# Performance work log

Hardware: AMD Instinct MI355X
Metric: run time of the kernel (lower is better)

The kernel has to match this reference:

```python
import jax, jax.numpy as jnp
import numpy as np

B, F, H, S, K, L, C = 128, 8192, 8192, 4, 32, 3, 100  # batch, encoded feats, hidden, segments, synapses/seg, hidden layers, classes


def setup_inputs() -> dict:
    key = jax.random.key(0)
    k1, k2, k3, k4, k5, k6 = jax.random.split(key, 6)
    # binary encoded input activations (thermometer-coded tabular features)
    x = jax.random.randint(k1, (B, F), 0, 2).astype(jnp.float32)
    # sign weights in {-1,+1} for each synapse of each segment of each neuron
    signs0 = jnp.where(jax.random.bernoulli(k2, 0.5, (S, H, K)), 1.0, -1.0).astype(jnp.float32)
    signsH = jnp.where(jax.random.bernoulli(k3, 0.5, (L - 1, S, H, K)), 1.0, -1.0).astype(jnp.float32)
    # synapse source indices (irregular connectivity)
    idx0 = jax.random.randint(k4, (S, H, K), 0, F, dtype=jnp.int32)
    idxH = jax.random.randint(k5, (L - 1, S, H, K), 0, H, dtype=jnp.int32)
    # per-layer output connection matrices [L, H, C]
    wout = jax.random.normal(k6, (L, H, C), dtype=jnp.float32) * 0.02
    return {"x": x, "signs0": signs0, "signsH": signsH, "wout": wout,
            "idx0": idx0, "idxH": idxH, "threshold": 8}


def _segment_layer(a, idx, signs, threshold):
    # a: [B, P] prev activations; idx/signs: [S, H, K]
    g = a[:, idx]                                  # [B, S, H, K] irregular gather
    z = jnp.einsum('bshk,shk->bsh', g, signs)      # per-segment summed input
    fired = jnp.any(z >= threshold, axis=1)        # OR over segments -> [B, H]
    return fired.astype(a.dtype)


def reference(x, signs0, signsH, wout, idx0, idxH, threshold):
    thr = jnp.float32(threshold)
    a = _segment_layer(x, idx0, signs0, thr)       # hidden layer 0
    acts = [a]
    for l in range(idxH.shape[0]):                 # remaining hidden layers (fixed small L)
        a = _segment_layer(a, idxH[l], signsH[l], thr)
        acts.append(a)
    # sum class votes from every hidden layer's output connection matrix
    out = jnp.einsum('lbh,lhc->bc', jnp.stack(acts, 0), wout)  # [B, C]
    return out
```

## Files before the change

kernel.cpp:

```cpp
#include <hip/hip_runtime.h>
#include <stdint.h>

#define B 128
#define F 8192
#define H 8192
#define S 4
#define K 32
#define L 3
#define C 100

__global__ void pack_x_kernel(const float* __restrict__ x, uint64_t* __restrict__ xP,
                              float* __restrict__ out) {
    const int zi = blockIdx.x * 128 + threadIdx.x;
    if (zi < B * C) out[zi] = 0.0f;

    const int b = threadIdx.x;
    const int w = threadIdx.x >> 6;
    const int f0 = blockIdx.x * 32;
    const float4* xr = (const float4*)(x + (size_t)b * F + f0);
    for (int j = 0; j < 8; ++j) {
        const float4 v = xr[j];
        const uint64_t m0 = __ballot(v.x > 0.5f);
        const uint64_t m1 = __ballot(v.y > 0.5f);
        const uint64_t m2 = __ballot(v.z > 0.5f);
        const uint64_t m3 = __ballot(v.w > 0.5f);
        if ((threadIdx.x & 63) == 0) {
            const int f = f0 + 4 * j;
            xP[(size_t)w * F + f + 0] = m0;
            xP[(size_t)w * F + f + 1] = m1;
            xP[(size_t)w * F + f + 2] = m2;
            xP[(size_t)w * F + f + 3] = m3;
        }
    }
}

__device__ __forceinline__ int load_threshold(const int* p) {
    int v = *p;
    if (v >= (1 << 23)) v = (int)__int_as_float(v);
    return v;
}

__global__ void layer_kernel(const uint64_t* __restrict__ prevP,
                             const int* __restrict__ idx,
                             const float* __restrict__ signs,
                             uint64_t* __restrict__ outP,
                             const int* __restrict__ thrp) {
    __shared__ uint64_t tab[H];
    const int tid  = threadIdx.x;
    const int lane = tid & 63;
    const int s    = tid >> 6;
    const int w    = blockIdx.x & 1;
    const int hg   = blockIdx.x >> 1;
    const int h    = hg * 64 + lane;
    const int thr  = load_threshold(thrp);

    {
        const ulonglong2* src = (const ulonglong2*)(prevP + (size_t)w * H);
        ulonglong2* dst = (ulonglong2*)tab;
#pragma unroll
        for (int i = 0; i < 16; ++i)
            dst[i * 256 + tid] = src[i * 256 + tid];
    }
    __syncthreads();

    uint64_t A[6] = {0, 0, 0, 0, 0, 0};
    uint64_t P[6] = {0, 0, 0, 0, 0, 0};
    const int4*   irow = (const int4*)(idx   + ((size_t)s * H + h) * K);
    const float4* srow = (const float4*)(signs + ((size_t)s * H + h) * K);
#pragma unroll
    for (int kk = 0; kk < 8; ++kk) {
        const int4   i4 = irow[kk];
        const float4 s4 = srow[kk];
        const int   iv[4] = {i4.x, i4.y, i4.z, i4.w};
        const float sv[4] = {s4.x, s4.y, s4.z, s4.w};
#pragma unroll
        for (int j = 0; j < 4; ++j) {
            const uint64_t a  = tab[iv[j]];
            const uint64_t pm = (uint64_t)(int64_t)(~(__float_as_int(sv[j]) >> 31));
            uint64_t c = a;
#pragma unroll
            for (int i = 0; i < 6; ++i) { const uint64_t t = A[i]; A[i] = t ^ c; c = t & c; }
            c = a & pm;
#pragma unroll
            for (int i = 0; i < 6; ++i) { const uint64_t t = P[i]; P[i] = t ^ c; c = t & c; }
        }
    }

    uint64_t Y[7];
    {
        uint64_t c = 0;
#pragma unroll
        for (int i = 0; i < 7; ++i) {
            const uint64_t ai = (i < 6) ? A[i] : 0ull;
            const uint64_t bm = ((thr >> i) & 1) ? ~0ull : 0ull;
            const uint64_t t  = ai ^ bm;
            Y[i] = t ^ c;
            c = (ai & bm) | (t & c);
        }
    }
    uint64_t bw = 0;
#pragma unroll
    for (int i = 0; i < 7; ++i) {
        const uint64_t x = (i >= 1) ? P[i - 1] : 0ull;
        const uint64_t d = x ^ Y[i];
        bw = ((~x) & Y[i]) | ((~d) & bw);
    }
    const uint64_t fired = ~bw;

    __syncthreads();
    uint64_t* fsbuf = tab;
    fsbuf[s * 64 + lane] = fired;
    __syncthreads();
    if (s == 0) {
        const uint64_t f = fsbuf[lane] | fsbuf[64 + lane] |
                           fsbuf[128 + lane] | fsbuf[192 + lane];
        outP[(size_t)w * H + h] = f;
    }
}

#define NHC 16
#define HCH (H / NHC)

__global__ void final_kernel(const uint64_t* __restrict__ actP,
                             const float* __restrict__ wout,
                             float* __restrict__ out) {
    const int lane = threadIdx.x & 63;
    const int wid  = threadIdx.x >> 6;
    const int hc   = blockIdx.x & (NHC - 1);
    const int bg   = blockIdx.x / NHC;
    const int b    = bg * 4 + wid;
    const int word = b >> 6;
    const int bit  = b & 63;

    float acc0 = 0.0f, acc1 = 0.0f;
    const int c1 = 64 + lane;
    const bool c1v = (c1 < C);

    for (int l = 0; l < L; ++l) {
        const uint64_t* aT = actP + ((size_t)l * 2 + word) * H;
        const float* wl = wout + (size_t)l * H * C;
        for (int r = 0; r < HCH / 64; ++r) {
            const int hbase = hc * HCH + r * 64;
            const uint64_t m = aT[hbase + lane];
            uint64_t hm = __ballot((m >> bit) & 1ull);
            while (hm) {
                const int slot = __ffsll((unsigned long long)hm) - 1;
                hm &= hm - 1;
                const float* wr = wl + (size_t)(hbase + slot) * C;
                acc0 += wr[lane];
                if (c1v) acc1 += wr[c1];
            }
        }
    }
    atomicAdd(&out[b * C + lane], acc0);
    if (c1v) atomicAdd(&out[b * C + c1], acc1);
}

extern "C" void kernel_launch(void* const* d_in, const int* in_sizes, int n_in,
                              void* d_out, int out_size, void* d_ws, size_t ws_size,
                              hipStream_t stream) {
    const float* x      = (const float*)d_in[0];
    const float* signs0 = (const float*)d_in[1];
    const float* signsH = (const float*)d_in[2];
    const float* wout   = (const float*)d_in[3];
    const int*   idx0   = (const int*)d_in[4];
    const int*   idxH   = (const int*)d_in[5];
    const int*   thr    = (const int*)d_in[6];
    float* out = (float*)d_out;

    uint64_t* xP   = (uint64_t*)d_ws;
    uint64_t* actP = xP + (size_t)2 * F;

    pack_x_kernel<<<F / 32, 128, 0, stream>>>(x, xP, out);

    layer_kernel<<<256, 256, 0, stream>>>(xP, idx0, signs0, actP, thr);
    layer_kernel<<<256, 256, 0, stream>>>(actP, idxH, signsH,
                                          actP + (size_t)2 * H, thr);
    layer_kernel<<<256, 256, 0, stream>>>(actP + (size_t)2 * H,
                                          idxH + (size_t)S * H * K,
                                          signsH + (size_t)S * H * K,
                                          actP + (size_t)4 * H, thr);

    final_kernel<<<32 * NHC, 256, 0, stream>>>(actP, wout, out);
}
```

Measured before the change: 129.1 us.

## Repack activations as 32-bit words and stage packed idx/sign rows in LDS

Bit-packed activations switch from two 64-bit batch words to four 32-bit words, which halves the per-block LDS table and doubles the layer grid from 256 to 512 blocks. Each block now loads its idx and sign rows cooperatively and coalesced, packs each sign bit into bit 31 of the index, and stores them in a padded LDS array. Threads then read from LDS instead of doing strided per-thread global loads, and they issue 8 gathers ahead of the popcount adders. The cost is that idx/sign global traffic is now repeated across the 4 batch-word blocks, and the bit-serial counter work is spread over twice as many blocks.

```diff
diff --git a/kernel.cpp b/kernel.cpp
--- a/kernel.cpp
+++ b/kernel.cpp
@@ -9,13 +9,13 @@
 #define L 3
 #define C 100
 
-__global__ void pack_x_kernel(const float* __restrict__ x, uint64_t* __restrict__ xP,
+__global__ void pack_x_kernel(const float* __restrict__ x, uint32_t* __restrict__ xP,
                               float* __restrict__ out) {
     const int zi = blockIdx.x * 128 + threadIdx.x;
     if (zi < B * C) out[zi] = 0.0f;
 
     const int b = threadIdx.x;
-    const int w = threadIdx.x >> 6;
+    const int wv = threadIdx.x >> 6;
     const int f0 = blockIdx.x * 32;
     const float4* xr = (const float4*)(x + (size_t)b * F + f0);
     for (int j = 0; j < 8; ++j) {
@@ -26,10 +26,12 @@
         const uint64_t m3 = __ballot(v.w > 0.5f);
         if ((threadIdx.x & 63) == 0) {
             const int f = f0 + 4 * j;
-            xP[(size_t)w * F + f + 0] = m0;
-            xP[(size_t)w * F + f + 1] = m1;
-            xP[(size_t)w * F + f + 2] = m2;
-            xP[(size_t)w * F + f + 3] = m3;
+            uint32_t* lo = xP + (size_t)(2 * wv) * F;
+            uint32_t* hi = xP + (size_t)(2 * wv + 1) * F;
+            lo[f + 0] = (uint32_t)m0;  hi[f + 0] = (uint32_t)(m0 >> 32);
+            lo[f + 1] = (uint32_t)m1;  hi[f + 1] = (uint32_t)(m1 >> 32);
+            lo[f + 2] = (uint32_t)m2;  hi[f + 2] = (uint32_t)(m2 >> 32);
+            lo[f + 3] = (uint32_t)m3;  hi[f + 3] = (uint32_t)(m3 >> 32);
         }
     }
 }
@@ -40,80 +42,100 @@
     return v;
 }
 
-__global__ void layer_kernel(const uint64_t* __restrict__ prevP,
+__global__ void layer_kernel(const uint32_t* __restrict__ prevP,
                              const int* __restrict__ idx,
                              const float* __restrict__ signs,
-                             uint64_t* __restrict__ outP,
+                             uint32_t* __restrict__ outP,
                              const int* __restrict__ thrp) {
-    __shared__ uint64_t tab[H];
+    __shared__ uint32_t tab[H];
+    __shared__ uint32_t isg[S][64 * 33];
+    __shared__ uint32_t fbuf[256];
     const int tid  = threadIdx.x;
     const int lane = tid & 63;
-    const int s    = tid >> 6;
-    const int w    = blockIdx.x & 1;
-    const int hg   = blockIdx.x >> 1;
+    const int sw   = tid >> 6;
+    const int w    = blockIdx.x & 3;
+    const int hg   = blockIdx.x >> 2;
     const int h    = hg * 64 + lane;
     const int thr  = load_threshold(thrp);
 
     {
-        const ulonglong2* src = (const ulonglong2*)(prevP + (size_t)w * H);
-        ulonglong2* dst = (ulonglong2*)tab;
-#pragma unroll
-        for (int i = 0; i < 16; ++i)
+        const int4* src = (const int4*)(prevP + (size_t)w * H);
+        int4* dst = (int4*)tab;
+#pragma unroll
+        for (int i = 0; i < 8; ++i)
             dst[i * 256 + tid] = src[i * 256 + tid];
     }
+    {
+        const int hrow = tid >> 2;
+        const int k0   = (tid & 3) * 8;
+#pragma unroll
+        for (int s = 0; s < S; ++s) {
+            const int4*   ib = (const int4*)(idx   + ((size_t)s * H + hg * 64) * K);
+            const float4* sb = (const float4*)(signs + ((size_t)s * H + hg * 64) * K);
+            const int4   ia = ib[2 * tid],     ic = ib[2 * tid + 1];
+            const float4 sa = sb[2 * tid],     sc = sb[2 * tid + 1];
+            uint32_t* dst = &isg[s][hrow * 33 + k0];
+            dst[0] = (uint32_t)ia.x | ((uint32_t)__float_as_int(sa.x) & 0x80000000u);
+            dst[1] = (uint32_t)ia.y | ((uint32_t)__float_as_int(sa.y) & 0x80000000u);
+            dst[2] = (uint32_t)ia.z | ((uint32_t)__float_as_int(sa.z) & 0x80000000u);
+            dst[3] = (uint32_t)ia.w | ((uint32_t)__float_as_int(sa.w) & 0x80000000u);
+            dst[4] = (uint32_t)ic.x | ((uint32_t)__float_as_int(sc.x) & 0x80000000u);
+            dst[5] = (uint32_t)ic.y | ((uint32_t)__float_as_int(sc.y) & 0x80000000u);
+            dst[6] = (uint32_t)ic.z | ((uint32_t)__float_as_int(sc.z) & 0x80000000u);
+            dst[7] = (uint32_t)ic.w | ((uint32_t)__float_as_int(sc.w) & 0x80000000u);
+        }
+    }
     __syncthreads();
 
-    uint64_t A[6] = {0, 0, 0, 0, 0, 0};
-    uint64_t P[6] = {0, 0, 0, 0, 0, 0};
-    const int4*   irow = (const int4*)(idx   + ((size_t)s * H + h) * K);
-    const float4* srow = (const float4*)(signs + ((size_t)s * H + h) * K);
-#pragma unroll
-    for (int kk = 0; kk < 8; ++kk) {
-        const int4   i4 = irow[kk];
-        const float4 s4 = srow[kk];
-        const int   iv[4] = {i4.x, i4.y, i4.z, i4.w};
-        const float sv[4] = {s4.x, s4.y, s4.z, s4.w};
-#pragma unroll
-        for (int j = 0; j < 4; ++j) {
-            const uint64_t a  = tab[iv[j]];
-            const uint64_t pm = (uint64_t)(int64_t)(~(__float_as_int(sv[j]) >> 31));
-            uint64_t c = a;
-#pragma unroll
-            for (int i = 0; i < 6; ++i) { const uint64_t t = A[i]; A[i] = t ^ c; c = t & c; }
-            c = a & pm;
-#pragma unroll
-            for (int i = 0; i < 6; ++i) { const uint64_t t = P[i]; P[i] = t ^ c; c = t & c; }
-        }
-    }
-
-    uint64_t Y[7];
+    uint32_t A[6] = {0, 0, 0, 0, 0, 0};
+    uint32_t P[6] = {0, 0, 0, 0, 0, 0};
+    const uint32_t* row = &isg[sw][lane * 33];
+#pragma unroll
+    for (int jc = 0; jc < K; jc += 8) {
+        uint32_t iv[8];
+#pragma unroll
+        for (int j = 0; j < 8; ++j) iv[j] = row[jc + j];
+        uint32_t a[8];
+#pragma unroll
+        for (int j = 0; j < 8; ++j) a[j] = tab[iv[j] & 0xFFFF];
+#pragma unroll
+        for (int j = 0; j < 8; ++j) {
+            const uint32_t pm = ~(uint32_t)((int32_t)iv[j] >> 31);
+            uint32_t c = a[j];
+#pragma unroll
+            for (int i = 0; i < 6; ++i) { const uint32_t t = A[i]; A[i] = t ^ c; c = t & c; }
+            c = a[j] & pm;
+#pragma unroll
+            for (int i = 0; i < 6; ++i) { const uint32_t t = P[i]; P[i] = t ^ c; c = t & c; }
+        }
+    }
+
+    uint32_t Y[7];
     {
-        uint64_t c = 0;
+        uint32_t c = 0;
 #pragma unroll
         for (int i = 0; i < 7; ++i) {
-            const uint64_t ai = (i < 6) ? A[i] : 0ull;
-            const uint64_t bm = ((thr >> i) & 1) ? ~0ull : 0ull;
-            const uint64_t t  = ai ^ bm;
+            const uint32_t ai = (i < 6) ? A[i] : 0u;
+            const uint32_t bm = ((thr >> i) & 1) ? 0xFFFFFFFFu : 0u;
+            const uint32_t t  = ai ^ bm;
             Y[i] = t ^ c;
             c = (ai & bm) | (t & c);
         }
     }
-    uint64_t bw = 0;
+    uint32_t bw = 0;
 #pragma unroll
     for (int i = 0; i < 7; ++i) {
-        const uint64_t x = (i >= 1) ? P[i - 1] : 0ull;
-        const uint64_t d = x ^ Y[i];
-        bw = ((~x) & Y[i]) | ((~d) & bw);
-    }
-    const uint64_t fired = ~bw;
-
+        const uint32_t xx = (i >= 1) ? P[i - 1] : 0u;
+        const uint32_t d  = xx ^ Y[i];
+        bw = ((~xx) & Y[i]) | ((~d) & bw);
+    }
+    const uint32_t fired = ~bw;
+
+    fbuf[sw * 64 + lane] = fired;
     __syncthreads();
-    uint64_t* fsbuf = tab;
-    fsbuf[s * 64 + lane] = fired;
-    __syncthreads();
-    if (s == 0) {
-        const uint64_t f = fsbuf[lane] | fsbuf[64 + lane] |
-                           fsbuf[128 + lane] | fsbuf[192 + lane];
+    if (sw == 0) {
+        const uint32_t f = fbuf[lane] | fbuf[64 + lane] |
+                           fbuf[128 + lane] | fbuf[192 + lane];
         outP[(size_t)w * H + h] = f;
     }
 }
@@ -121,7 +143,7 @@
 #define NHC 16
 #define HCH (H / NHC)
 
-__global__ void final_kernel(const uint64_t* __restrict__ actP,
+__global__ void final_kernel(const uint32_t* __restrict__ actP,
                              const float* __restrict__ wout,
                              float* __restrict__ out) {
     const int lane = threadIdx.x & 63;
@@ -129,20 +151,20 @@
     const int hc   = blockIdx.x & (NHC - 1);
     const int bg   = blockIdx.x / NHC;
     const int b    = bg * 4 + wid;
-    const int word = b >> 6;
-    const int bit  = b & 63;
+    const int w32  = b >> 5;
+    const int bit  = b & 31;
 
     float acc0 = 0.0f, acc1 = 0.0f;
     const int c1 = 64 + lane;
     const bool c1v = (c1 < C);
 
     for (int l = 0; l < L; ++l) {
-        const uint64_t* aT = actP + ((size_t)l * 2 + word) * H;
+        const uint32_t* aT = actP + ((size_t)l * 4 + w32) * H;
         const float* wl = wout + (size_t)l * H * C;
         for (int r = 0; r < HCH / 64; ++r) {
             const int hbase = hc * HCH + r * 64;
-            const uint64_t m = aT[hbase + lane];
-            uint64_t hm = __ballot((m >> bit) & 1ull);
+            const uint32_t m = aT[hbase + lane];
+            uint64_t hm = __ballot((m >> bit) & 1u);
             while (hm) {
                 const int slot = __ffsll((unsigned long long)hm) - 1;
                 hm &= hm - 1;
@@ -168,18 +190,18 @@
     const int*   thr    = (const int*)d_in[6];
     float* out = (float*)d_out;
 
-    uint64_t* xP   = (uint64_t*)d_ws;
-    uint64_t* actP = xP + (size_t)2 * F;
+    uint32_t* xP   = (uint32_t*)d_ws;
+    uint32_t* actP = xP + (size_t)4 * F;
 
     pack_x_kernel<<<F / 32, 128, 0, stream>>>(x, xP, out);
 
-    layer_kernel<<<256, 256, 0, stream>>>(xP, idx0, signs0, actP, thr);
-    layer_kernel<<<256, 256, 0, stream>>>(actP, idxH, signsH,
-                                          actP + (size_t)2 * H, thr);
-    layer_kernel<<<256, 256, 0, stream>>>(actP + (size_t)2 * H,
+    layer_kernel<<<512, 256, 0, stream>>>(xP, idx0, signs0, actP, thr);
+    layer_kernel<<<512, 256, 0, stream>>>(actP, idxH, signsH,
+                                          actP + (size_t)4 * H, thr);
+    layer_kernel<<<512, 256, 0, stream>>>(actP + (size_t)4 * H,
                                           idxH + (size_t)S * H * K,
                                           signsH + (size_t)S * H * K,
-                                          actP + (size_t)4 * H, thr);
+                                          actP + (size_t)8 * H, thr);
 
     final_kernel<<<32 * NHC, 256, 0, stream>>>(actP, wout, out);
 }
```

Result: no change. 130.7 us (+1.2%).
